# Optimization experiments

Measured on AMD Instinct MI355X. Metric: run time of the kernel, lower is better.

Reference implementation:

```python
import jax, jax.numpy as jnp
import numpy as np
import math

_LINK_MASK_VALUE = -1000000000.0
B, N, HID, NH = 8, 1024, 1024, 4
HD = HID // NH


def setup_inputs() -> dict:
    key = jax.random.key(0)
    ks = jax.random.split(key, 8)
    features = jax.random.normal(ks[0], (B, N, HID), dtype=jnp.float32)
    valid_mask = jax.random.bernoulli(ks[1], 0.9, (B, N))
    s = 0.02
    Wq = jax.random.normal(ks[2], (HID, HID), dtype=jnp.float32) * s
    bq = jnp.zeros((HID,), dtype=jnp.float32)
    Wk = jax.random.normal(ks[3], (HID, HID), dtype=jnp.float32) * s
    bk = jnp.zeros((HID,), dtype=jnp.float32)
    Wg = jax.random.normal(ks[4], (HID, NH), dtype=jnp.float32) * s
    bg = jnp.zeros((NH,), dtype=jnp.float32)
    return {"features": features, "valid_mask": valid_mask,
            "Wq": Wq, "bq": bq, "Wk": Wk, "bk": bk, "Wg": Wg, "bg": bg}


def reference(features, valid_mask, Wq, bq, Wk, bk, Wg, bg):
    b, n, _ = features.shape
    Q = (features @ Wq + bq).reshape(b, n, NH, HD)
    K = (features @ Wk + bk).reshape(b, n, NH, HD)
    log_gates = jax.nn.log_softmax(features @ Wg + bg, axis=-1)  # (b, n, H)
    scores = jnp.einsum('bihd,bjhd->bijh', Q, K) / math.sqrt(HD)  # (b, i, j, H)
    triu = jnp.triu(jnp.ones((n, n), dtype=bool), k=1)            # (n, n)
    tvm = triu[None, :, :] & valid_mask[:, None, :]               # (b, i, j)
    row_dead = ~jnp.any(tvm, axis=2, keepdims=True)               # (b, i, 1)
    tvm = tvm | row_dead
    scores = jnp.where(tvm[..., None], scores, _LINK_MASK_VALUE)
    log_per_head = jax.nn.log_softmax(scores, axis=2)             # softmax over j
    log_per_head = jnp.where(row_dead[..., None], _LINK_MASK_VALUE, log_per_head)
    # mixture over heads with per-row gates
    log_links = jax.scipy.special.logsumexp(log_per_head + log_gates[:, :, None, :], axis=-1)
    return log_links
```

## Files before the change

### kernel.cpp

```cpp
#include <hip/hip_runtime.h>


typedef __attribute__((ext_vector_type(8))) short bf16x8;
typedef __attribute__((ext_vector_type(4))) short bf16x4;
typedef __attribute__((ext_vector_type(4))) float f32x4;
typedef __attribute__((ext_vector_type(16))) float f32x16;
typedef __attribute__((ext_vector_type(8))) int i32x8;

#define LB __launch_bounds__(256)

__device__ __forceinline__ short f2bf(float f) {
    unsigned u = __float_as_uint(f);
    u += 0x7fffu + ((u >> 16) & 1u);
    return (short)(u >> 16);
}

__device__ __forceinline__ void gld16(const void* g, void* l) {
    __builtin_amdgcn_global_load_lds(
        (const __attribute__((address_space(1))) unsigned int*)g,
        (__attribute__((address_space(3))) unsigned int*)l, 16, 0, 0);
}

__global__ LB void k_prep2(const float* __restrict__ feat, const float* __restrict__ Wg,
                           const float* __restrict__ bg, const float* __restrict__ Wq,
                           const float* __restrict__ Wk, char* __restrict__ X8,
                           float* __restrict__ lgA, char* __restrict__ W8) {
    __shared__ float tile[32][33];
    const int t = threadIdx.x;
    if (blockIdx.x < 2048) {
        int row = blockIdx.x * 4 + (t >> 6);
        int lane = t & 63;
        const float* f = feat + (size_t)row * 1024;
        float g0 = 0.f, g1 = 0.f, g2 = 0.f, g3 = 0.f;
#pragma unroll
        for (int tt = 0; tt < 4; ++tt) {
            int k = tt * 256 + lane * 4;
            float4 x = *(const float4*)&f[k];
            float4 w0 = *(const float4*)&Wg[(k + 0) * 4];
            float4 w1 = *(const float4*)&Wg[(k + 1) * 4];
            float4 w2 = *(const float4*)&Wg[(k + 2) * 4];
            float4 w3 = *(const float4*)&Wg[(k + 3) * 4];
            g0 += x.x * w0.x + x.y * w1.x + x.z * w2.x + x.w * w3.x;
            g1 += x.x * w0.y + x.y * w1.y + x.z * w2.y + x.w * w3.y;
            g2 += x.x * w0.z + x.y * w1.z + x.z * w2.z + x.w * w3.z;
            g3 += x.x * w0.w + x.y * w1.w + x.z * w2.w + x.w * w3.w;
            unsigned u01 = (unsigned)__builtin_amdgcn_cvt_pk_fp8_f32(x.x, x.y, 0, false);
            unsigned u23 = (unsigned)__builtin_amdgcn_cvt_pk_fp8_f32(x.z, x.w, 0, false);
            *(unsigned*)&X8[(size_t)row * 1024 + k] = (u01 & 0xffffu) | (u23 << 16);
        }
#pragma unroll
        for (int off = 32; off; off >>= 1) {
            g0 += __shfl_xor(g0, off); g1 += __shfl_xor(g1, off);
            g2 += __shfl_xor(g2, off); g3 += __shfl_xor(g3, off);
        }
        g0 += bg[0]; g1 += bg[1]; g2 += bg[2]; g3 += bg[3];
        float m = fmaxf(fmaxf(g0, g1), fmaxf(g2, g3));
        float s = __expf(g0 - m) + __expf(g1 - m) + __expf(g2 - m) + __expf(g3 - m);
        float ls = m + __logf(s);
        if (lane == 0) {
            float4 o = {g0 - ls, g1 - ls, g2 - ls, g3 - ls};
            *(float4*)&lgA[row * 4] = o;
        }
    } else {
        int bid = blockIdx.x - 2048;
        int n0 = (bid & 63) * 32, k0 = (bid >> 6) * 32;
        const float* W = (n0 < 1024) ? Wq : Wk;
        int nb = n0 & 1023;
        int tx = t & 31, ty = t >> 5;
#pragma unroll
        for (int jj = 0; jj < 4; ++jj) {
            int k = ty + jj * 8;
            tile[k][tx] = W[(size_t)(k0 + k) * 1024 + nb + tx];
        }
        __syncthreads();
#pragma unroll
        for (int jj = 0; jj < 4; ++jj) {
            int n = ty + jj * 8;
            float w16 = tile[tx][n] * 16.f;
            W8[(size_t)(n0 + n) * 1024 + k0 + tx] =
                (char)(__builtin_amdgcn_cvt_pk_fp8_f32(w16, w16, 0, false) & 0xff);
        }
    }
}

__device__ __forceinline__ i32x8 ldfrag8(const char* tb, int row, int khalf) {
    const int sw = (row >> 1) & 3;
    uint4 lo = *(const uint4*)&tb[row * 64 + (((khalf * 2 + 0) ^ sw) * 16)];
    uint4 hi = *(const uint4*)&tb[row * 64 + (((khalf * 2 + 1) ^ sw) * 16)];
    i32x8 r;
    r[0] = lo.x; r[1] = lo.y; r[2] = lo.z; r[3] = lo.w;
    r[4] = hi.x; r[5] = hi.y; r[6] = hi.z; r[7] = hi.w;
    return r;
}

__global__ __launch_bounds__(512, 2) void k_gemm(const char* __restrict__ X8,
                                                 const char* __restrict__ W8,
                                                 const float* __restrict__ bq,
                                                 const float* __restrict__ bk,
                                                 char* __restrict__ Q8,
                                                 char* __restrict__ K8) {
    __shared__ char SM[3][32768];
    const int t = threadIdx.x;
    const int lane = t & 63, wid = t >> 6;
    const int wr = wid >> 2, wc = wid & 3;
    const int l31 = lane & 31, khalf = lane >> 5;
    const int wgid = (blockIdx.x & 7) * 32 + (blockIdx.x >> 3);
    const int m0t = (wgid >> 3) * 256, n0t = (wgid & 7) * 256;

    f32x16 acc[4][2] = {};

#define SGA(q, k1, dst)                                                         \
    { int s_ = (q) * 512 + t; int tr_ = s_ >> 2, c_ = s_ & 3;                   \
      gld16(&X8[(size_t)(m0t + tr_) * 1024 + (k1) + (((c_) ^ ((tr_ >> 1) & 3)) * 16)], \
            (dst) + s_ * 16); }
#define SGB(q, k1, dst)                                                         \
    { int s_ = (q) * 512 + t; int tr_ = s_ >> 2, c_ = s_ & 3;                   \
      gld16(&W8[(size_t)(n0t + tr_) * 1024 + (k1) + (((c_) ^ ((tr_ >> 1) & 3)) * 16)], \
            (dst) + 16384 + s_ * 16); }

    SGA(0, 0, SM[0]); SGA(1, 0, SM[0]); SGB(0, 0, SM[0]); SGB(1, 0, SM[0]);
    SGA(0, 64, SM[1]); SGA(1, 64, SM[1]); SGB(0, 64, SM[1]); SGB(1, 64, SM[1]);
    asm volatile("s_waitcnt vmcnt(4)" ::: "memory");
    __builtin_amdgcn_sched_barrier(0);
    __builtin_amdgcn_s_barrier();

    for (int kt = 0; kt < 16; ++kt) {
        const char* buf = SM[kt % 3];
        char* bufn = SM[(kt + 2) % 3];
        if (kt < 14) {
            const int k2 = (kt + 2) * 64;
            SGA(0, k2, bufn); SGA(1, k2, bufn); SGB(0, k2, bufn); SGB(1, k2, bufn);
        }
        i32x8 aF[4], bF[2];
#pragma unroll
        for (int rt = 0; rt < 4; ++rt)
            aF[rt] = ldfrag8(buf, wr * 128 + rt * 32 + l31, khalf);
#pragma unroll
        for (int ct = 0; ct < 2; ++ct)
            bF[ct] = ldfrag8(buf + 16384, wc * 64 + ct * 32 + l31, khalf);
        __builtin_amdgcn_s_setprio(1);
#pragma unroll
        for (int rt = 0; rt < 4; ++rt)
#pragma unroll
            for (int ct = 0; ct < 2; ++ct)
                acc[rt][ct] = __builtin_amdgcn_mfma_scale_f32_32x32x64_f8f6f4(
                    aF[rt], bF[ct], acc[rt][ct], 0, 0, 0, 127, 0, 127);
        __builtin_amdgcn_s_setprio(0);
        if (kt < 14)       asm volatile("s_waitcnt vmcnt(4)" ::: "memory");
        else if (kt == 14) asm volatile("s_waitcnt vmcnt(0)" ::: "memory");
        __builtin_amdgcn_sched_barrier(0);
        __builtin_amdgcn_s_barrier();
    }
#undef SGA
#undef SGB

#pragma unroll
    for (int rt = 0; rt < 4; ++rt) {
#pragma unroll
        for (int ct = 0; ct < 2; ++ct) {
            const int col = n0t + wc * 64 + ct * 32 + l31;
            const float bias = (col < 1024) ? bq[col] : bk[col - 1024];
            char* dst = (col < 1024) ? Q8 : K8;
            const int h = (col >> 8) & 3, d = col & 255;
#pragma unroll
            for (int reg = 0; reg < 16; ++reg) {
                const int rin = (reg & 3) + 8 * (reg >> 2) + 4 * khalf;
                const int grow = m0t + wr * 128 + rt * 32 + rin;
                const int b_ = grow >> 10, i_ = grow & 1023;
                float v = acc[rt][ct][reg] * 0.0625f + bias;
                dst[((size_t)(b_ * 4 + h) * 1024 + i_) * 256 + d] =
                    (char)(__builtin_amdgcn_cvt_pk_fp8_f32(v, v, 0, false) & 0xff);
            }
        }
    }
}

__device__ __forceinline__ i32x8 ldsc(const char* tb, int row, int p0) {
    const int sw = row & 15;
    uint4 lo = *(const uint4*)&tb[row * 256 + (((p0 + 0) ^ sw) * 16)];
    uint4 hi = *(const uint4*)&tb[row * 256 + (((p0 + 1) ^ sw) * 16)];
    i32x8 r;
    r[0] = lo.x; r[1] = lo.y; r[2] = lo.z; r[3] = lo.w;
    r[4] = hi.x; r[5] = hi.y; r[6] = hi.z; r[7] = hi.w;
    return r;
}

__global__ __launch_bounds__(256, 2) void k_sc(const char* __restrict__ Q8,
                                               const char* __restrict__ K8,
                                               const int* __restrict__ vm,
                                               char* __restrict__ Pe8,
                                               float* __restrict__ Zp) {
    __shared__ char SMEM[65536];
    char* As = SMEM;
    char* Bs = SMEM + 32768;
    const int t = threadIdx.x;
    const int lane = t & 63, wid = t >> 6;
    const int wr = wid >> 1, wc = wid & 1;
    const int l31 = lane & 31, khalf = lane >> 5;
    const int gidx = (blockIdx.x & 7) * 144 + (blockIdx.x >> 3);
    const int bh = gidx / 36, tt = gidx % 36;
    const int it8 = (tt >= 8) + (tt >= 15) + (tt >= 21) + (tt >= 26)
                  + (tt >= 30) + (tt >= 33) + (tt >= 35);
    const int base8 = (it8 == 0) ? 0 : (it8 == 1) ? 8 : (it8 == 2) ? 15
                    : (it8 == 3) ? 21 : (it8 == 4) ? 26 : (it8 == 5) ? 30
                    : (it8 == 6) ? 33 : 35;
    const int jt8 = it8 + (tt - base8);
    const int b = bh >> 2;
    const char* Qp = Q8 + ((size_t)bh << 18);
    const char* Kp = K8 + ((size_t)bh << 18);

#pragma unroll
    for (int pass = 0; pass < 8; ++pass) {
        int s_ = pass * 256 + t;
        int row = s_ >> 4, g = s_ & 15;
        gld16(&Qp[(size_t)(it8 * 128 + row) * 256 + ((g ^ (row & 15)) * 16)],
              As + s_ * 16);
    }
#pragma unroll
    for (int pass = 0; pass < 8; ++pass) {
        int s_ = pass * 256 + t;
        int row = s_ >> 4, g = s_ & 15;
        gld16(&Kp[(size_t)(jt8 * 128 + row) * 256 + ((g ^ (row & 15)) * 16)],
              Bs + s_ * 16);
    }
    asm volatile("s_waitcnt vmcnt(0)" ::: "memory");
    __builtin_amdgcn_sched_barrier(0);
    __builtin_amdgcn_s_barrier();

    f32x16 acc[2][2] = {};
#pragma unroll
    for (int ks = 0; ks < 4; ++ks) {
        const int p0 = ks * 4 + khalf * 2;
        i32x8 aF[2], bF[2];
#pragma unroll
        for (int rt = 0; rt < 2; ++rt)
            aF[rt] = ldsc(As, wr * 64 + rt * 32 + l31, p0);
#pragma unroll
        for (int ct = 0; ct < 2; ++ct)
            bF[ct] = ldsc(Bs, wc * 64 + ct * 32 + l31, p0);
        __builtin_amdgcn_s_setprio(1);
#pragma unroll
        for (int rt = 0; rt < 2; ++rt)
#pragma unroll
            for (int ct = 0; ct < 2; ++ct)
                acc[rt][ct] = __builtin_amdgcn_mfma_scale_f32_32x32x64_f8f6f4(
                    aF[rt], bF[ct], acc[rt][ct], 0, 0, 0, 127, 0, 127);
        __builtin_amdgcn_s_setprio(0);
    }

    __syncthreads();
    char* wbuf = SMEM + wid * 5120;
    char* Pp = Pe8 + ((size_t)bh << 20);
    const int rowbase = it8 * 128 + wr * 64;
    const int colbase = jt8 * 128 + wc * 64;
    int vmv[2];
#pragma unroll
    for (int ct = 0; ct < 2; ++ct)
        vmv[ct] = vm[(b << 10) + colbase + ct * 32 + l31];
    float zacc[2][16] = {};
#pragma unroll
    for (int rt = 0; rt < 2; ++rt) {
#pragma unroll
        for (int ct = 0; ct < 2; ++ct) {
            const int col = colbase + ct * 32 + l31;
#pragma unroll
            for (int reg = 0; reg < 16; ++reg) {
                const int rin = (reg & 3) + 8 * (reg >> 2) + 4 * khalf;
                const int row = rowbase + rt * 32 + rin;
                float e = __expf(acc[rt][ct][reg] * 0.0625f);
                zacc[rt][reg] += (vmv[ct] && (col > row)) ? e : 0.f;
                wbuf[(rt * 32 + rin) * 80 + ct * 32 + l31] =
                    (char)(__builtin_amdgcn_cvt_pk_fp8_f32(e, e, 0, false) & 0xff);
            }
        }
    }
#pragma unroll
    for (int c = 0; c < 4; ++c) {
        const int rrow = c * 16 + (lane >> 2);
        uint4 v = *(const uint4*)&wbuf[rrow * 80 + (lane & 3) * 16];
        const int grow = rowbase + rrow;
        if (colbase + 63 > grow)
            *(uint4*)&Pp[(size_t)grow * 1024 + colbase + (lane & 3) * 16] = v;
    }
#pragma unroll
    for (int rt = 0; rt < 2; ++rt)
#pragma unroll
        for (int reg = 0; reg < 16; ++reg) {
            zacc[rt][reg] += __shfl_xor(zacc[rt][reg], 1);
            zacc[rt][reg] += __shfl_xor(zacc[rt][reg], 2);
            zacc[rt][reg] += __shfl_xor(zacc[rt][reg], 4);
            zacc[rt][reg] += __shfl_xor(zacc[rt][reg], 8);
            zacc[rt][reg] += __shfl_xor(zacc[rt][reg], 16);
        }
    if (l31 == 0) {
        float* Zs = Zp + (size_t)(jt8 * 2 + wc) * 32768 + bh * 1024;
#pragma unroll
        for (int rt = 0; rt < 2; ++rt)
#pragma unroll
            for (int reg = 0; reg < 16; ++reg) {
                const int rin = (reg & 3) + 8 * (reg >> 2) + 4 * khalf;
                Zs[rowbase + rt * 32 + rin] = zacc[rt][reg];
            }
    }
}

__global__ LB void k_final(const char* __restrict__ Pe8, const int* __restrict__ vm,
                           const float* __restrict__ lgA, const float* __restrict__ Zp,
                           float* __restrict__ out) {
    __shared__ float ecs[4];
    const int blk = blockIdx.x;
    const int b = blk >> 10, i = blk & 1023;
    const int t = threadIdx.x;
    if (t < 64) {
        int h = t >> 4, sl = t & 15;
        int base = (b * 4 + h) * 1024 + i;
        float z = (sl >= ((i >> 7) << 1)) ? Zp[(size_t)sl * 32768 + base] : 0.f;
        z += __shfl_xor(z, 1); z += __shfl_xor(z, 2);
        z += __shfl_xor(z, 4); z += __shfl_xor(z, 8);
        if (sl == 0) {
            float lgv = lgA[blk * 4 + h];
            ecs[h] = (z > 0.f) ? __expf(lgv) / z : 0.f;
        }
    }
    __syncthreads();
    const int j0 = t * 4;
    float4 o = {-1.0e9f, -1.0e9f, -1.0e9f, -1.0e9f};
    if (j0 + 3 > i) {
        int4 v4 = *(const int4*)&vm[(b << 10) + j0];
        float a0 = 0.f, a1 = 0.f, a2 = 0.f, a3 = 0.f;
#pragma unroll
        for (int h = 0; h < 4; ++h) {
            unsigned p = *(const unsigned*)
                &Pe8[(((size_t)(b * 4 + h)) << 20) + ((size_t)i << 10) + j0];
            float ech = ecs[h];
            a0 += __builtin_amdgcn_cvt_f32_fp8((int)p, 0) * ech;
            a1 += __builtin_amdgcn_cvt_f32_fp8((int)p, 1) * ech;
            a2 += __builtin_amdgcn_cvt_f32_fp8((int)p, 2) * ech;
            a3 += __builtin_amdgcn_cvt_f32_fp8((int)p, 3) * ech;
        }
        o.x = (v4.x && (j0 + 0 > i)) ? __logf(a0) : -1.0e9f;
        o.y = (v4.y && (j0 + 1 > i)) ? __logf(a1) : -1.0e9f;
        o.z = (v4.z && (j0 + 2 > i)) ? __logf(a2) : -1.0e9f;
        o.w = (v4.w && (j0 + 3 > i)) ? __logf(a3) : -1.0e9f;
    }
    *(float4*)&out[((size_t)blk << 10) + j0] = o;
}

extern "C" void kernel_launch(void* const* d_in, const int* in_sizes, int n_in,
                              void* d_out, int out_size, void* d_ws, size_t ws_size,
                              hipStream_t stream) {
    const float* features = (const float*)d_in[0];
    const int*   vmask    = (const int*)d_in[1];
    const float* Wq       = (const float*)d_in[2];
    const float* bq       = (const float*)d_in[3];
    const float* Wk       = (const float*)d_in[4];
    const float* bk       = (const float*)d_in[5];
    const float* Wg       = (const float*)d_in[6];
    const float* bg       = (const float*)d_in[7];
    float* out = (float*)d_out;

    char*  Pe8 = (char*)d_ws;
    char*  X8  = (char*)d_ws;
    char*  W8  = X8 + 8388608;
    char*  Q8  = (char*)d_ws + 33554432;
    char*  K8  = Q8 + 8388608;
    float* lgA = (float*)(K8 + 8388608);
    float* Zp  = lgA + 32768;

    k_prep2<<<4096, 256, 0, stream>>>(features, Wg, bg, Wq, Wk, X8, lgA, W8);
    k_gemm<<<256, 512, 0, stream>>>(X8, W8, bq, bk, Q8, K8);
    k_sc<<<1152, 256, 0, stream>>>(Q8, K8, vmask, Pe8, Zp);
    k_final<<<8192, 256, 0, stream>>>(Pe8, vmask, lgA, Zp, out);
}
```

Measured before the change: 76.58 us.

## Recompute scores in output pass instead of materializing fp8 probability matrix

Rather than writing the exponentiated scores as an fp8 matrix and reading it back in a final pass, the score kernel now only produces the row partition sums. A tiny kernel turns those sums into per-head gate/normalizer factors. A new output kernel recomputes QK^T for all four heads per tile with MFMA and mixes them in registers before taking the log. This drops the large intermediate write and read at the cost of running the score GEMM twice, and the output stores are scattered per-lane scalar writes rather than coalesced float4.

```diff
diff --git a/kernel.cpp b/kernel.cpp
--- a/kernel.cpp
+++ b/kernel.cpp
@@ -1,19 +1,11 @@
 #include <hip/hip_runtime.h>
 
 
-typedef __attribute__((ext_vector_type(8))) short bf16x8;
-typedef __attribute__((ext_vector_type(4))) short bf16x4;
 typedef __attribute__((ext_vector_type(4))) float f32x4;
 typedef __attribute__((ext_vector_type(16))) float f32x16;
 typedef __attribute__((ext_vector_type(8))) int i32x8;
 
 #define LB __launch_bounds__(256)
-
-__device__ __forceinline__ short f2bf(float f) {
-    unsigned u = __float_as_uint(f);
-    u += 0x7fffu + ((u >> 16) & 1u);
-    return (short)(u >> 16);
-}
 
 __device__ __forceinline__ void gld16(const void* g, void* l) {
     __builtin_amdgcn_global_load_lds(
@@ -185,11 +177,10 @@
     return r;
 }
 
-__global__ __launch_bounds__(256, 2) void k_sc(const char* __restrict__ Q8,
-                                               const char* __restrict__ K8,
-                                               const int* __restrict__ vm,
-                                               char* __restrict__ Pe8,
-                                               float* __restrict__ Zp) {
+__global__ __launch_bounds__(256, 2) void k_z(const char* __restrict__ Q8,
+                                              const char* __restrict__ K8,
+                                              const int* __restrict__ vm,
+                                              float* __restrict__ Zp) {
     __shared__ char SMEM[65536];
     char* As = SMEM;
     char* Bs = SMEM + 32768;
@@ -248,9 +239,6 @@
         __builtin_amdgcn_s_setprio(0);
     }
 
-    __syncthreads();
-    char* wbuf = SMEM + wid * 5120;
-    char* Pp = Pe8 + ((size_t)bh << 20);
     const int rowbase = it8 * 128 + wr * 64;
     const int colbase = jt8 * 128 + wc * 64;
     int vmv[2];
@@ -259,7 +247,7 @@
         vmv[ct] = vm[(b << 10) + colbase + ct * 32 + l31];
     float zacc[2][16] = {};
 #pragma unroll
-    for (int rt = 0; rt < 2; ++rt) {
+    for (int rt = 0; rt < 2; ++rt)
 #pragma unroll
         for (int ct = 0; ct < 2; ++ct) {
             const int col = colbase + ct * 32 + l31;
@@ -269,19 +257,8 @@
                 const int row = rowbase + rt * 32 + rin;
                 float e = __expf(acc[rt][ct][reg] * 0.0625f);
                 zacc[rt][reg] += (vmv[ct] && (col > row)) ? e : 0.f;
-                wbuf[(rt * 32 + rin) * 80 + ct * 32 + l31] =
-                    (char)(__builtin_amdgcn_cvt_pk_fp8_f32(e, e, 0, false) & 0xff);
             }
         }
-    }
-#pragma unroll
-    for (int c = 0; c < 4; ++c) {
-        const int rrow = c * 16 + (lane >> 2);
-        uint4 v = *(const uint4*)&wbuf[rrow * 80 + (lane & 3) * 16];
-        const int grow = rowbase + rrow;
-        if (colbase + 63 > grow)
-            *(uint4*)&Pp[(size_t)grow * 1024 + colbase + (lane & 3) * 16] = v;
-    }
 #pragma unroll
     for (int rt = 0; rt < 2; ++rt)
 #pragma unroll
@@ -304,46 +281,136 @@
     }
 }
 
-__global__ LB void k_final(const char* __restrict__ Pe8, const int* __restrict__ vm,
-                           const float* __restrict__ lgA, const float* __restrict__ Zp,
-                           float* __restrict__ out) {
-    __shared__ float ecs[4];
-    const int blk = blockIdx.x;
-    const int b = blk >> 10, i = blk & 1023;
+__global__ LB void k_c(const float* __restrict__ lgA, const float* __restrict__ Zp,
+                       float* __restrict__ ecF) {
+    int idx = blockIdx.x * 256 + threadIdx.x;
+    int b = idx >> 10, i = idx & 1023;
+    int sl0 = (i >> 7) * 2;
+    float4 lg = *(const float4*)&lgA[idx * 4];
+    float4 o;
+#pragma unroll
+    for (int h = 0; h < 4; ++h) {
+        int base = (b * 4 + h) * 1024 + i;
+        float Zv = 0.f;
+        for (int sl = sl0; sl < 16; ++sl) Zv += Zp[sl * 32768 + base];
+        float lgv = (h == 0) ? lg.x : (h == 1) ? lg.y : (h == 2) ? lg.z : lg.w;
+        float e = (Zv > 0.f) ? __expf(lgv) / Zv : 0.f;
+        if (h == 0) o.x = e; else if (h == 1) o.y = e;
+        else if (h == 2) o.z = e; else o.w = e;
+    }
+    *(float4*)&ecF[idx * 4] = o;
+}
+
+__global__ __launch_bounds__(256, 2) void k_out(const char* __restrict__ Q8,
+                                                const char* __restrict__ K8,
+                                                const int* __restrict__ vm,
+                                                const float* __restrict__ ecF,
+                                                float* __restrict__ out) {
+    __shared__ char SMEM[65536];
+    __shared__ float ecL[4][128];
+    char* As = SMEM;
+    char* Bs = SMEM + 32768;
     const int t = threadIdx.x;
-    if (t < 64) {
-        int h = t >> 4, sl = t & 15;
-        int base = (b * 4 + h) * 1024 + i;
-        float z = (sl >= ((i >> 7) << 1)) ? Zp[(size_t)sl * 32768 + base] : 0.f;
-        z += __shfl_xor(z, 1); z += __shfl_xor(z, 2);
-        z += __shfl_xor(z, 4); z += __shfl_xor(z, 8);
-        if (sl == 0) {
-            float lgv = lgA[blk * 4 + h];
-            ecs[h] = (z > 0.f) ? __expf(lgv) / z : 0.f;
-        }
-    }
-    __syncthreads();
-    const int j0 = t * 4;
-    float4 o = {-1.0e9f, -1.0e9f, -1.0e9f, -1.0e9f};
-    if (j0 + 3 > i) {
-        int4 v4 = *(const int4*)&vm[(b << 10) + j0];
-        float a0 = 0.f, a1 = 0.f, a2 = 0.f, a3 = 0.f;
-#pragma unroll
-        for (int h = 0; h < 4; ++h) {
-            unsigned p = *(const unsigned*)
-                &Pe8[(((size_t)(b * 4 + h)) << 20) + ((size_t)i << 10) + j0];
-            float ech = ecs[h];
-            a0 += __builtin_amdgcn_cvt_f32_fp8((int)p, 0) * ech;
-            a1 += __builtin_amdgcn_cvt_f32_fp8((int)p, 1) * ech;
-            a2 += __builtin_amdgcn_cvt_f32_fp8((int)p, 2) * ech;
-            a3 += __builtin_amdgcn_cvt_f32_fp8((int)p, 3) * ech;
-        }
-        o.x = (v4.x && (j0 + 0 > i)) ? __logf(a0) : -1.0e9f;
-        o.y = (v4.y && (j0 + 1 > i)) ? __logf(a1) : -1.0e9f;
-        o.z = (v4.z && (j0 + 2 > i)) ? __logf(a2) : -1.0e9f;
-        o.w = (v4.w && (j0 + 3 > i)) ? __logf(a3) : -1.0e9f;
-    }
-    *(float4*)&out[((size_t)blk << 10) + j0] = o;
+    const int lane = t & 63, wid = t >> 6;
+    const int wr = wid >> 1, wc = wid & 1;
+    const int l31 = lane & 31, khalf = lane >> 5;
+    const int b = blockIdx.x & 7;
+    const int tile = blockIdx.x >> 3;
+    const int it8 = tile >> 3, jt8 = tile & 7;
+    const int i0blk = it8 * 128, j0blk = jt8 * 128;
+
+    if (jt8 < it8) {
+        const float4 m4 = {-1.0e9f, -1.0e9f, -1.0e9f, -1.0e9f};
+#pragma unroll
+        for (int pass = 0; pass < 16; ++pass) {
+            int s_ = pass * 256 + t;
+            int r = s_ >> 5, cg = s_ & 31;
+            *(float4*)&out[((size_t)((b << 10) + i0blk + r) << 10) + j0blk + cg * 4] = m4;
+        }
+        return;
+    }
+
+    if (t < 128) {
+        float4 e = *(const float4*)&ecF[((b << 10) + i0blk + t) * 4];
+        ecL[0][t] = e.x; ecL[1][t] = e.y; ecL[2][t] = e.z; ecL[3][t] = e.w;
+    }
+
+    float aex[2][2][16] = {};
+    for (int h = 0; h < 4; ++h) {
+        const char* Qp = Q8 + ((size_t)(b * 4 + h) << 18);
+        const char* Kp = K8 + ((size_t)(b * 4 + h) << 18);
+#pragma unroll
+        for (int pass = 0; pass < 8; ++pass) {
+            int s_ = pass * 256 + t;
+            int row = s_ >> 4, g = s_ & 15;
+            gld16(&Qp[(size_t)(i0blk + row) * 256 + ((g ^ (row & 15)) * 16)],
+                  As + s_ * 16);
+        }
+#pragma unroll
+        for (int pass = 0; pass < 8; ++pass) {
+            int s_ = pass * 256 + t;
+            int row = s_ >> 4, g = s_ & 15;
+            gld16(&Kp[(size_t)(j0blk + row) * 256 + ((g ^ (row & 15)) * 16)],
+                  Bs + s_ * 16);
+        }
+        asm volatile("s_waitcnt vmcnt(0)" ::: "memory");
+        __builtin_amdgcn_sched_barrier(0);
+        __builtin_amdgcn_s_barrier();
+
+        f32x16 acc[2][2] = {};
+#pragma unroll
+        for (int ks = 0; ks < 4; ++ks) {
+            const int p0 = ks * 4 + khalf * 2;
+            i32x8 aF[2], bF[2];
+#pragma unroll
+            for (int rt = 0; rt < 2; ++rt)
+                aF[rt] = ldsc(As, wr * 64 + rt * 32 + l31, p0);
+#pragma unroll
+            for (int ct = 0; ct < 2; ++ct)
+                bF[ct] = ldsc(Bs, wc * 64 + ct * 32 + l31, p0);
+            __builtin_amdgcn_s_setprio(1);
+#pragma unroll
+            for (int rt = 0; rt < 2; ++rt)
+#pragma unroll
+                for (int ct = 0; ct < 2; ++ct)
+                    acc[rt][ct] = __builtin_amdgcn_mfma_scale_f32_32x32x64_f8f6f4(
+                        aF[rt], bF[ct], acc[rt][ct], 0, 0, 0, 127, 0, 127);
+            __builtin_amdgcn_s_setprio(0);
+        }
+#pragma unroll
+        for (int rt = 0; rt < 2; ++rt)
+#pragma unroll
+            for (int ct = 0; ct < 2; ++ct)
+#pragma unroll
+                for (int reg = 0; reg < 16; ++reg) {
+                    const int rin = (reg & 3) + 8 * (reg >> 2) + 4 * khalf;
+                    const int rloc = wr * 64 + rt * 32 + rin;
+                    aex[rt][ct][reg] += __expf(acc[rt][ct][reg] * 0.0625f)
+                                        * ecL[h][rloc];
+                }
+        __syncthreads();
+    }
+
+    const int rowbase = wr * 64;
+    const int colbase = j0blk + wc * 64;
+    int vmv[2];
+#pragma unroll
+    for (int ct = 0; ct < 2; ++ct)
+        vmv[ct] = vm[(b << 10) + colbase + ct * 32 + l31];
+#pragma unroll
+    for (int rt = 0; rt < 2; ++rt)
+#pragma unroll
+        for (int ct = 0; ct < 2; ++ct) {
+            const int col = colbase + ct * 32 + l31;
+#pragma unroll
+            for (int reg = 0; reg < 16; ++reg) {
+                const int rin = (reg & 3) + 8 * (reg >> 2) + 4 * khalf;
+                const int gi = i0blk + rowbase + rt * 32 + rin;
+                float o = (vmv[ct] && (col > gi)) ? __logf(aex[rt][ct][reg])
+                                                  : -1.0e9f;
+                out[((size_t)((b << 10) + gi) << 10) + col] = o;
+            }
+        }
 }
 
 extern "C" void kernel_launch(void* const* d_in, const int* in_sizes, int n_in,
@@ -359,16 +426,17 @@
     const float* bg       = (const float*)d_in[7];
     float* out = (float*)d_out;
 
-    char*  Pe8 = (char*)d_ws;
     char*  X8  = (char*)d_ws;
     char*  W8  = X8 + 8388608;
-    char*  Q8  = (char*)d_ws + 33554432;
+    char*  Q8  = W8 + 2097152;
     char*  K8  = Q8 + 8388608;
     float* lgA = (float*)(K8 + 8388608);
     float* Zp  = lgA + 32768;
+    float* ecF = Zp + 524288;
 
     k_prep2<<<4096, 256, 0, stream>>>(features, Wg, bg, Wq, Wk, X8, lgA, W8);
     k_gemm<<<256, 512, 0, stream>>>(X8, W8, bq, bk, Q8, K8);
-    k_sc<<<1152, 256, 0, stream>>>(Q8, K8, vmask, Pe8, Zp);
-    k_final<<<8192, 256, 0, stream>>>(Pe8, vmask, lgA, Zp, out);
-}
+    k_z<<<1152, 256, 0, stream>>>(Q8, K8, vmask, Zp);
+    k_c<<<32, 256, 0, stream>>>(lgA, Zp, ecF);
+    k_out<<<512, 256, 0, stream>>>(Q8, K8, vmask, ecF, out);
+}
```

Measured after the change: 94.52 us. 23.4% more time.
